# Performance work log

Measured on AMD Instinct MI355X. Metric: run time of the kernel, lower is better.

Reference implementation:

```python
import jax, jax.numpy as jnp
import numpy as np

H = 384          # hidden_dim == filter_size == n_chans
N_BINS = 256
PRED_GRAD = 0.1
LN_EPS = 1e-5


def _conv1d_same(x_bct, w_oik, b):
    k = w_oik.shape[-1]
    p = (k - 1) // 2
    y = jax.lax.conv_general_dilated(
        x_bct, w_oik, window_strides=(1,), padding=[(p, p)],
        dimension_numbers=("NCT", "OIT", "NCT"))
    return y + b[None, :, None]


def _ln_last(x, g, b):  # LayerNorm over last dim
    m = jnp.mean(x, axis=-1, keepdims=True)
    v = jnp.var(x, axis=-1, keepdims=True)
    return (x - m) * jax.lax.rsqrt(v + LN_EPS) * g + b


def _ln_chan(x_bct, g, b):  # LayerNorm over channel dim (dim=1)
    m = jnp.mean(x_bct, axis=1, keepdims=True)
    v = jnp.var(x_bct, axis=1, keepdims=True)
    return (x_bct - m) * jax.lax.rsqrt(v + LN_EPS) * g[None, :, None] + b[None, :, None]


def _sin_pos(x0, dim):
    # fairseq SinusoidalPositionalEmbedding, padding_idx=0, applied to xs[...,0]
    mask = (x0 != 0).astype(jnp.int32)
    pos = jnp.cumsum(mask, axis=1) * mask                        # [B,T]
    half = dim // 2
    inv = jnp.exp(jnp.arange(half, dtype=jnp.float32) * (-(np.log(10000.0) / (half - 1))))
    ang = pos[..., None].astype(jnp.float32) * inv               # [B,T,half]
    pe = jnp.concatenate([jnp.sin(ang), jnp.cos(ang)], axis=-1)  # [B,T,dim]
    return jnp.where(pos[..., None] == 0, 0.0, pe)


def _duration_predictor(x, src_mask, w1, b1, g1, be1, w2, b2, g2, be2, lw, lb):
    h = _conv1d_same(jnp.swapaxes(x, 1, 2), w1, b1)
    h = _ln_last(jax.nn.relu(jnp.swapaxes(h, 1, 2)), g1, be1)
    h = _conv1d_same(jnp.swapaxes(h, 1, 2), w2, b2)
    h = _ln_last(jax.nn.relu(jnp.swapaxes(h, 1, 2)), g2, be2)
    out = (h @ lw + lb)[..., 0]                                  # [B,T]
    return jnp.where(src_mask, 0.0, out)


def _variance_predictor(x, cw, cb, g, b, lw, lb, alpha):
    pos = alpha * _sin_pos(x[..., 0], x.shape[-1])
    h = jnp.swapaxes(x + pos, 1, 2)                              # [B,C,T]
    for i in range(cw.shape[0]):
        h = _ln_chan(jax.nn.relu(_conv1d_same(h, cw[i], cb[i])), g[i], b[i])
    return jnp.swapaxes(h, 1, 2) @ lw + lb                       # [B,T,odim]


def _length_regulate(x, dur_int, max_len):
    B, T, _ = x.shape
    cum = jnp.cumsum(dur_int, axis=1)                            # [B,T]
    frames = jnp.arange(max_len)
    idx = jax.vmap(lambda c: jnp.searchsorted(c, frames, side="right"))(cum)
    idx = jnp.clip(idx, 0, T - 1)                                # [B,max_len]
    out = jnp.take_along_axis(x, idx[..., None], axis=1)         # [B,max_len,H]
    total = cum[:, -1]
    valid = frames[None, :] < total[:, None]
    out = jnp.where(valid[..., None], out, 0.0)
    mel_len = jnp.minimum(total, max_len)
    return out, mel_len


def setup_inputs() -> dict:
    key = jax.random.key(0)
    ks = iter(jax.random.split(key, 40))
    B, T = 32, 1024
    rnd = lambda s: 0.02 * jax.random.normal(next(ks), s, dtype=jnp.float32)
    inp = {
        "x": jax.random.normal(next(ks), (B, T, H), dtype=jnp.float32),
        "src_lens": jax.random.randint(next(ks), (B,), 0, T),
        "src_mask": jnp.zeros((B, T), dtype=bool),
        "max_len": 4096,
        # duration predictor (kernel=3)
        "dp_w1": rnd((H, H, 3)), "dp_b1": jnp.zeros((H,)),
        "dp_ln1_g": jnp.ones((H,)), "dp_ln1_b": jnp.zeros((H,)),
        "dp_w2": rnd((H, H, 3)), "dp_b2": jnp.zeros((H,)),
        "dp_ln2_g": jnp.ones((H,)), "dp_ln2_b": jnp.zeros((H,)),
        "dp_lw": rnd((H, 1)), "dp_lb": jnp.full((1,), 1.5),  # bias -> avg dur ~3.5
        # pitch predictor: 5 layers, kernel=5, odim=1 (use_uv=False)
        "pp_cw": rnd((5, H, H, 5)), "pp_cb": jnp.zeros((5, H)),
        "pp_g": jnp.ones((5, H)), "pp_b": jnp.zeros((5, H)),
        "pp_lw": rnd((H, 1)), "pp_lb": jnp.zeros((1,)), "pp_alpha": jnp.ones((1,)),
        # energy predictor: 2 layers, kernel=5, odim=1
        "ep_cw": rnd((2, H, H, 5)), "ep_cb": jnp.zeros((2, H)),
        "ep_g": jnp.ones((2, H)), "ep_b": jnp.zeros((2, H)),
        "ep_lw": rnd((H, 1)), "ep_lb": jnp.zeros((1,)), "ep_alpha": jnp.ones((1,)),
        # bins (requires_grad=False buffers) + embedding tables
        "pitch_bins": jnp.linspace(-4.0, 4.0, N_BINS - 1),
        "energy_bins": jnp.linspace(-4.0, 4.0, N_BINS - 1),
        "pitch_table": rnd((N_BINS, H)),
        "energy_table": rnd((N_BINS, H)),
    }
    return inp


def reference(x, src_lens, src_mask, max_len,
              dp_w1, dp_b1, dp_ln1_g, dp_ln1_b, dp_w2, dp_b2, dp_ln2_g, dp_ln2_b, dp_lw, dp_lb,
              pp_cw, pp_cb, pp_g, pp_b, pp_lw, pp_lb, pp_alpha,
              ep_cw, ep_cb, ep_g, ep_b, ep_lw, ep_lb, ep_alpha,
              pitch_bins, energy_bins, pitch_table, energy_table):
    # duration (inference path: no targets, controls = 1.0)
    log_d = _duration_predictor(x, src_mask, dp_w1, dp_b1, dp_ln1_g, dp_ln1_b,
                                dp_w2, dp_b2, dp_ln2_g, dp_ln2_b, dp_lw, dp_lb)
    dur = jnp.clip(jnp.round(jnp.exp(log_d) - 1.0), 0.0, None)
    dur_int = dur.astype(jnp.int32)

    # straight-through-style grad scaling on predictor inputs
    xg = jax.lax.stop_gradient(x) + PRED_GRAD * (x - jax.lax.stop_gradient(x))

    # phoneme-level pitch (use_uv=False -> squeeze, bucketize)
    pitch_pred = _variance_predictor(xg, pp_cw, pp_cb, pp_g, pp_b, pp_lw, pp_lb, pp_alpha)[..., 0]
    pitch_idx = jnp.searchsorted(pitch_bins, pitch_pred, side="left")  # torch.bucketize(right=False)
    pitch_emb = pitch_table[pitch_idx]

    # phoneme-level energy
    energy_pred = _variance_predictor(xg, ep_cw, ep_cb, ep_g, ep_b, ep_lw, ep_lb, ep_alpha)[..., 0]
    energy_idx = jnp.searchsorted(energy_bins, energy_pred, side="left")
    energy_emb = energy_table[energy_idx]

    x_adapt = x + pitch_emb + energy_emb
    out, mel_len = _length_regulate(x_adapt, dur_int, int(max_len))
    return out, log_d, dur, pitch_pred, energy_pred, mel_len
```

## Files before the change

kernel.cpp:

```cpp
#include <hip/hip_runtime.h>
#include <cstdint>

#define HH 384
#define NBINS 256

typedef __attribute__((ext_vector_type(8))) short short8v;
typedef __attribute__((ext_vector_type(16))) float f32x16;
typedef __attribute__((ext_vector_type(4))) unsigned short ushort4v;

__device__ inline float4 ld4(const float* p){ return *(const float4*)p; }

__device__ inline unsigned short bf16_rne(float f){
  unsigned u = __float_as_uint(f);
  unsigned r = u + 0x7FFFu + ((u >> 16) & 1u);
  return (unsigned short)(r >> 16);
}
__device__ inline float bf16_to_f(unsigned short h){
  return __uint_as_float(((unsigned)h) << 16);
}

__global__ __launch_bounds__(1024) void pos_kernel(const float* __restrict__ x,
    int* __restrict__ pos, int T)
{
  __shared__ int s[1024];
  int b = blockIdx.x, tid = threadIdx.x;
  int m = 0;
  if (tid < T) m = (x[((size_t)b*T + tid)*HH] != 0.f) ? 1 : 0;
  s[tid] = m;
  __syncthreads();
  for (int off = 1; off < 1024; off <<= 1){
    int add = (tid >= off) ? s[tid-off] : 0;
    __syncthreads();
    s[tid] += add;
    __syncthreads();
  }
  if (tid < T) pos[(size_t)b*T + tid] = s[tid] * m;
}

__global__ __launch_bounds__(HH) void add_pe_kernel(const float* __restrict__ x,
    const int* __restrict__ pos, const float* __restrict__ alpha,
    float* __restrict__ out)
{
  int row = blockIdx.x; int i = threadIdx.x;
  int p = pos[row];
  float pe = 0.f;
  if (p != 0){
    int j = (i < HH/2) ? i : i - HH/2;
    float inv = expf((float)j * -0.04822167734018944f);
    float ang = (float)p * inv;
    pe = (i < HH/2) ? sinf(ang) : cosf(ang);
  }
  out[(size_t)row*HH + i] = x[(size_t)row*HH + i] + alpha[0]*pe;
}

template<int K>
__global__ __launch_bounds__(256) void wtrans_kernel(const float* __restrict__ w,
    unsigned short* __restrict__ dst, int nlayers)
{
  constexpr int SPL = (24*K + 2) * 6144;
  const int per = 384*384;
  int gid = blockIdx.x*256 + threadIdx.x;
  if (gid >= nlayers*per) return;
  int l = gid / per, rem = gid - l*per;
  int o = rem / 384, i = rem - (rem/384)*384;
  unsigned short* whi = dst + (size_t)l*2*SPL;
  unsigned short* wlo = whi + SPL;
  const float* wl = w + (size_t)l*384*384*K;
  int ph = (i >= 192) ? 1 : 0;
  int iloc = i - 192*ph;
  int c = iloc >> 4, half = (iloc >> 3) & 1, jj = iloc & 7;
  #pragma unroll
  for (int k = 0; k < K; ++k){
    float v = wl[((size_t)o*384 + i)*K + k];
    unsigned short hi = bf16_rne(v);
    unsigned short lo = bf16_rne(v - bf16_to_f(hi));
    int s = ph*12*K + k*12 + c;
    size_t d = ((size_t)(s*2 + half)*384 + o)*8 + jj;
    whi[d] = hi; wlo[d] = lo;
  }
}

template<int K>
__global__ __launch_bounds__(256) void conv_mfma_kernel(
    const float* __restrict__ in, const unsigned short* __restrict__ whi,
    const unsigned short* __restrict__ wlo, const float* __restrict__ bias,
    const float* __restrict__ g, const float* __restrict__ be,
    float* __restrict__ out, int T)
{
  constexpr int MT  = 64;
  constexpr int P   = (K-1)/2;
  constexpr int RT  = MT + K - 1;
  constexpr int RA  = RT + 2;
  constexpr int SPH = 12*K;
  constexpr int LDPc = 200;
  __shared__ unsigned short xs_hi[RA*LDPc];
  __shared__ unsigned short xs_lo[RA*LDPc];
  __shared__ float ps[4][64], pq[4][64];

  int ntile = T / MT;
  int b  = blockIdx.x / ntile;
  int t0 = (blockIdx.x % ntile) * MT;
  int tid = threadIdx.x;
  const float* inb = in + (size_t)b*T*HH;

  int wv = tid >> 6, ln = tid & 63;
  int l31 = ln & 31, hl = ln >> 5;
  int o0 = wv * 96;

  f32x16 acc0[3], acc1[3];
  #pragma unroll
  for (int nt = 0; nt < 3; ++nt){
    float bv = bias[o0 + nt*32 + l31];
    #pragma unroll
    for (int r = 0; r < 16; ++r){ acc0[nt][r] = bv; acc1[nt][r] = bv; }
  }

#define GLOAD(dst, p) \
  asm volatile("global_load_dwordx4 %0, %1, off" : "=v"(dst) : "v"(p))

  for (int phse = 0; phse < 2; ++phse){
    if (phse) __syncthreads();

    for (int e4 = tid; e4 < RT*48; e4 += 256){
      int r = e4 / 48, c4 = (e4 - r*48)*4;
      int t = t0 + r - P;
      float4 v = (t >= 0 && t < T) ? ld4(&inb[(size_t)t*HH + phse*192 + c4])
                                   : make_float4(0.f,0.f,0.f,0.f);
      float va[4] = {v.x, v.y, v.z, v.w};
      ushort4v h, l;
      #pragma unroll
      for (int q = 0; q < 4; ++q){
        unsigned short hq = bf16_rne(va[q]);
        h[q] = hq;
        l[q] = bf16_rne(va[q] - bf16_to_f(hq));
      }
      *(ushort4v*)&xs_hi[r*LDPc + c4] = h;
      *(ushort4v*)&xs_lo[r*LDPc + c4] = l;
    }
    __syncthreads();

    const unsigned short* bhp = whi + (size_t)phse*SPH*6144
                                    + ((size_t)hl*384 + o0 + l31)*8;
    const unsigned short* blp = wlo + (size_t)phse*SPH*6144
                                    + ((size_t)hl*384 + o0 + l31)*8;
    int aoff0 = l31*LDPc + hl*8;
    int aoff1 = (32 + l31)*LDPc + hl*8;
    int cc = 0;

    short8v B0h[3], B0l[3], B1h[3], B1l[3];
    short8v A00h, A00l, A01h, A01l;
    short8v A10h, A10l, A11h, A11l;

#define ADVB do{ bhp += 6144; blp += 6144; }while(0)
#define ADVA do{ aoff0 += 16; aoff1 += 16;                                   \
                 if (++cc == 12){ cc = 0; aoff0 += LDPc - 192;               \
                                  aoff1 += LDPc - 192; } }while(0)

    GLOAD(B0h[0], bhp);        GLOAD(B0h[1], bhp + 256); GLOAD(B0h[2], bhp + 512);
    GLOAD(B0l[0], blp);        GLOAD(B0l[1], blp + 256); GLOAD(B0l[2], blp + 512);
    ADVB;
    A00h = *(const short8v*)&xs_hi[aoff0];
    A00l = *(const short8v*)&xs_lo[aoff0];
    A01h = *(const short8v*)&xs_hi[aoff1];
    A01l = *(const short8v*)&xs_lo[aoff1];
    ADVA;

#define STEP(CBh,CBl, CA0h,CA0l,CA1h,CA1l, NBh,NBl, NA0h,NA0l,NA1h,NA1l) do{ \
    GLOAD(NBh[0], bhp);       GLOAD(NBh[1], bhp + 256);                      \
    GLOAD(NBh[2], bhp + 512); GLOAD(NBl[0], blp);                            \
    GLOAD(NBl[1], blp + 256); GLOAD(NBl[2], blp + 512);                      \
    ADVB;                                                                    \
    NA0h = *(const short8v*)&xs_hi[aoff0];                                   \
    NA0l = *(const short8v*)&xs_lo[aoff0];                                   \
    NA1h = *(const short8v*)&xs_hi[aoff1];                                   \
    NA1l = *(const short8v*)&xs_lo[aoff1];                                   \
    ADVA;                                                                    \
    asm volatile("s_waitcnt vmcnt(6)");                                      \
    __builtin_amdgcn_sched_barrier(0);                                       \
    __builtin_amdgcn_s_setprio(1);                                           \
    _Pragma("unroll")                                                        \
    for (int nt = 0; nt < 3; ++nt){                                          \
      acc0[nt] = __builtin_amdgcn_mfma_f32_32x32x16_bf16(CA0h, CBh[nt], acc0[nt], 0,0,0); \
      acc1[nt] = __builtin_amdgcn_mfma_f32_32x32x16_bf16(CA1h, CBh[nt], acc1[nt], 0,0,0); \
    }                                                                        \
    _Pragma("unroll")                                                        \
    for (int nt = 0; nt < 3; ++nt){                                          \
      acc0[nt] = __builtin_amdgcn_mfma_f32_32x32x16_bf16(CA0h, CBl[nt], acc0[nt], 0,0,0); \
      acc1[nt] = __builtin_amdgcn_mfma_f32_32x32x16_bf16(CA1h, CBl[nt], acc1[nt], 0,0,0); \
    }                                                                        \
    _Pragma("unroll")                                                        \
    for (int nt = 0; nt < 3; ++nt){                                          \
      acc0[nt] = __builtin_amdgcn_mfma_f32_32x32x16_bf16(CA0l, CBh[nt], acc0[nt], 0,0,0); \
      acc1[nt] = __builtin_amdgcn_mfma_f32_32x32x16_bf16(CA1l, CBh[nt], acc1[nt], 0,0,0); \
    }                                                                        \
    __builtin_amdgcn_s_setprio(0);                                           \
  } while(0)

    for (int s = 0; s < SPH; s += 2){
      STEP(B0h,B0l, A00h,A00l,A01h,A01l, B1h,B1l, A10h,A10l,A11h,A11l);
      STEP(B1h,B1l, A10h,A10l,A11h,A11l, B0h,B0l, A00h,A00l,A01h,A01l);
    }
#undef STEP
#undef ADVB
#undef ADVA

    asm volatile("s_waitcnt vmcnt(0)");
    __builtin_amdgcn_sched_barrier(0);
  }
#undef GLOAD

  float gv[3], bev[3];
  #pragma unroll
  for (int nt = 0; nt < 3; ++nt){
    gv[nt]  = g[o0 + nt*32 + l31];
    bev[nt] = be[o0 + nt*32 + l31];
  }

  #pragma unroll
  for (int rg = 0; rg < 2; ++rg){
    #pragma unroll
    for (int r = 0; r < 16; ++r){
      float s1 = 0.f, s2 = 0.f;
      #pragma unroll
      for (int nt = 0; nt < 3; ++nt){
        float v = fmaxf(rg ? acc1[nt][r] : acc0[nt][r], 0.f);
        if (rg) acc1[nt][r] = v; else acc0[nt][r] = v;
        s1 += v; s2 += v*v;
      }
      s1 += __shfl_xor(s1, 1);  s2 += __shfl_xor(s2, 1);
      s1 += __shfl_xor(s1, 2);  s2 += __shfl_xor(s2, 2);
      s1 += __shfl_xor(s1, 4);  s2 += __shfl_xor(s2, 4);
      s1 += __shfl_xor(s1, 8);  s2 += __shfl_xor(s2, 8);
      s1 += __shfl_xor(s1, 16); s2 += __shfl_xor(s2, 16);
      if (l31 == 0){
        int t = rg*32 + (r&3) + 8*(r>>2) + 4*hl;
        ps[wv][t] = s1; pq[wv][t] = s2;
      }
    }
  }
  __syncthreads();

  #pragma unroll
  for (int rg = 0; rg < 2; ++rg){
    #pragma unroll
    for (int r = 0; r < 16; ++r){
      int t = rg*32 + (r&3) + 8*(r>>2) + 4*hl;
      float s1 = ps[0][t] + ps[1][t] + ps[2][t] + ps[3][t];
      float s2 = pq[0][t] + pq[1][t] + pq[2][t] + pq[3][t];
      float mn  = s1 * (1.f/HH);
      float var = fmaxf(s2 * (1.f/HH) - mn*mn, 0.f);
      float rr  = rsqrtf(var + 1e-5f);
      float* orow = out + ((size_t)b*T + t0 + t)*HH;
      #pragma unroll
      for (int nt = 0; nt < 3; ++nt){
        float v = rg ? acc1[nt][r] : acc0[nt][r];
        orow[o0 + nt*32 + l31] = (v - mn)*rr*gv[nt] + bev[nt];
      }
    }
  }
}

__global__ __launch_bounds__(256) void proj_var_kernel(const float* __restrict__ h,
    const float* __restrict__ lw, const float* __restrict__ lb,
    const float* __restrict__ bins, float* __restrict__ pred,
    int* __restrict__ idx, int nrows)
{
  int lane = threadIdx.x & 63, wid = threadIdx.x >> 6;
  int wave = blockIdx.x*4 + wid, nw = gridDim.x*4;
  float lwr[6];
  #pragma unroll
  for (int j = 0; j < 6; ++j) lwr[j] = lw[lane + 64*j];
  float lbv = lb[0];
  for (int row = wave; row < nrows; row += nw){
    const float* hr = h + (size_t)row*HH;
    float s = 0.f;
    #pragma unroll
    for (int j = 0; j < 6; ++j) s = fmaf(hr[lane + 64*j], lwr[j], s);
    #pragma unroll
    for (int off = 32; off; off >>= 1) s += __shfl_xor(s, off);
    if (lane == 0){
      float v = s + lbv;
      pred[row] = v;
      int lo = 0, hi = NBINS - 1;
      while (lo < hi){ int mid = (lo + hi) >> 1; if (bins[mid] < v) lo = mid + 1; else hi = mid; }
      idx[row] = lo;
    }
  }
}

__global__ __launch_bounds__(256) void proj_dur_kernel(const float* __restrict__ h,
    const float* __restrict__ lw, const float* __restrict__ lb,
    const unsigned char* __restrict__ mask, float* __restrict__ logd,
    float* __restrict__ durf, int* __restrict__ duri, int nrows)
{
  int lane = threadIdx.x & 63, wid = threadIdx.x >> 6;
  int wave = blockIdx.x*4 + wid, nw = gridDim.x*4;
  float lwr[6];
  #pragma unroll
  for (int j = 0; j < 6; ++j) lwr[j] = lw[lane + 64*j];
  float lbv = lb[0];
  for (int row = wave; row < nrows; row += nw){
    const float* hr = h + (size_t)row*HH;
    float s = 0.f;
    #pragma unroll
    for (int j = 0; j < 6; ++j) s = fmaf(hr[lane + 64*j], lwr[j], s);
    #pragma unroll
    for (int off = 32; off; off >>= 1) s += __shfl_xor(s, off);
    if (lane == 0){
      float v = s + lbv;
      if (mask[row]) v = 0.f;
      logd[row] = v;
      float d = fmaxf(rintf(expf(v) - 1.f), 0.f);
      durf[row] = d;
      duri[row] = (int)d;
    }
  }
}

__global__ __launch_bounds__(1024) void cumsum_kernel(const int* __restrict__ duri,
    int* __restrict__ cum, float* __restrict__ mel, int T, int ML)
{
  __shared__ int s[1024];
  int b = blockIdx.x, tid = threadIdx.x;
  s[tid] = (tid < T) ? duri[(size_t)b*T + tid] : 0;
  __syncthreads();
  for (int off = 1; off < 1024; off <<= 1){
    int add = (tid >= off) ? s[tid-off] : 0;
    __syncthreads();
    s[tid] += add;
    __syncthreads();
  }
  if (tid < T) cum[(size_t)b*T + tid] = s[tid];
  if (tid == T-1) mel[b] = (float)min(s[tid], ML);
}

__global__ __launch_bounds__(256) void xadapt_kernel(const float* __restrict__ x,
    const int* __restrict__ ip, const int* __restrict__ ie,
    const float* __restrict__ pt, const float* __restrict__ et,
    float* __restrict__ xa, int nrows)
{
  int gid = blockIdx.x*256 + threadIdx.x;
  int n4 = nrows * (HH/4);
  if (gid >= n4) return;
  int row = gid / (HH/4);
  int c = gid - row*(HH/4);
  float4 xv = ((const float4*)x)[gid];
  const float4* pr = (const float4*)(pt + (size_t)ip[row]*HH);
  const float4* er = (const float4*)(et + (size_t)ie[row]*HH);
  float4 pv = pr[c], ev = er[c];
  ((float4*)xa)[gid] = make_float4(xv.x+pv.x+ev.x, xv.y+pv.y+ev.y,
                                   xv.z+pv.z+ev.z, xv.w+pv.w+ev.w);
}

__global__ __launch_bounds__(256) void lr_kernel(const float* __restrict__ xa,
    const int* __restrict__ cum, float* __restrict__ out, int T, int ML)
{
  constexpr int FR = 32;
  __shared__ int scum[1024];
  __shared__ int sidx[FR];
  __shared__ int svalid[FR];
  int b  = blockIdx.y;
  int f0 = blockIdx.x * FR;
  for (int i = threadIdx.x; i < T; i += 256) scum[i] = cum[(size_t)b*T + i];
  __syncthreads();
  int total = scum[T-1];
  if (threadIdx.x < FR){
    int f = f0 + threadIdx.x;
    int lo = 0, hi = T;
    while (lo < hi){ int mid = (lo + hi) >> 1; if (scum[mid] <= f) lo = mid + 1; else hi = mid; }
    sidx[threadIdx.x] = min(lo, T-1);
    svalid[threadIdx.x] = (f < total) ? 1 : 0;
  }
  __syncthreads();
  #pragma unroll
  for (int it = 0; it < FR*(HH/4)/256; ++it){
    int item = it*256 + threadIdx.x;
    int fl = item / (HH/4);
    int c  = item - fl*(HH/4);
    int f  = f0 + fl;
    if (f >= ML) continue;
    float4 v = make_float4(0.f,0.f,0.f,0.f);
    if (svalid[fl]) v = ((const float4*)(xa + ((size_t)b*T + sidx[fl])*HH))[c];
    ((float4*)(out + ((size_t)b*ML + f)*HH))[c] = v;
  }
}

extern "C" void kernel_launch(void* const* d_in, const int* in_sizes, int n_in,
                              void* d_out, int out_size, void* d_ws, size_t ws_size,
                              hipStream_t stream)
{
  const float* x        = (const float*)d_in[0];
  const unsigned char* src_mask = (const unsigned char*)d_in[2];
  const float* dp_w1 = (const float*)d_in[4];
  const float* dp_b1 = (const float*)d_in[5];
  const float* dp_g1 = (const float*)d_in[6];
  const float* dp_be1= (const float*)d_in[7];
  const float* dp_w2 = (const float*)d_in[8];
  const float* dp_b2 = (const float*)d_in[9];
  const float* dp_g2 = (const float*)d_in[10];
  const float* dp_be2= (const float*)d_in[11];
  const float* dp_lw = (const float*)d_in[12];
  const float* dp_lb = (const float*)d_in[13];
  const float* pp_cw = (const float*)d_in[14];
  const float* pp_cb = (const float*)d_in[15];
  const float* pp_g  = (const float*)d_in[16];
  const float* pp_b  = (const float*)d_in[17];
  const float* pp_lw = (const float*)d_in[18];
  const float* pp_lb = (const float*)d_in[19];
  const float* pp_alpha = (const float*)d_in[20];
  const float* ep_cw = (const float*)d_in[21];
  const float* ep_cb = (const float*)d_in[22];
  const float* ep_g  = (const float*)d_in[23];
  const float* ep_b  = (const float*)d_in[24];
  const float* ep_lw = (const float*)d_in[25];
  const float* ep_lb = (const float*)d_in[26];
  const float* ep_alpha = (const float*)d_in[27];
  const float* pbins = (const float*)d_in[28];
  const float* ebins = (const float*)d_in[29];
  const float* ptab  = (const float*)d_in[30];
  const float* etab  = (const float*)d_in[31];

  int B = in_sizes[1];
  int T = in_sizes[0] / (B*HH);
  int ML = (int)(((long long)out_size - B - 4LL*B*T) / ((long long)B*HH));
  size_t rows = (size_t)B*T;

  float* bufA = (float*)d_ws;
  float* bufB = bufA + rows*HH;
  int* pos    = (int*)(bufB + rows*HH);
  int* idx_p  = pos + rows;
  int* idx_e  = idx_p + rows;
  int* dur_i  = idx_e + rows;
  int* cum    = dur_i + rows;

  float* out0    = (float*)d_out;
  float* logd    = out0 + (size_t)B*ML*HH;
  float* durf    = logd + rows;
  float* pitchp  = durf + rows;
  float* energyp = pitchp + rows;
  float* mel     = energyp + rows;

  const size_t SPL5 = (size_t)(24*5 + 2)*6144;
  const size_t SPL3 = (size_t)(24*3 + 2)*6144;
  unsigned short* wsc    = (unsigned short*)d_out;
  unsigned short* pitchW = wsc;
  unsigned short* enerW  = pitchW + 5*2*SPL5;
  unsigned short* durW1  = enerW  + 2*2*SPL5;
  unsigned short* durW2  = durW1  + 2*SPL3;

  const int per = 384*384;
  wtrans_kernel<5><<<(5*per + 255)/256, 256, 0, stream>>>(pp_cw, pitchW, 5);
  wtrans_kernel<5><<<(2*per + 255)/256, 256, 0, stream>>>(ep_cw, enerW, 2);
  wtrans_kernel<3><<<(per + 255)/256, 256, 0, stream>>>(dp_w1, durW1, 1);
  wtrans_kernel<3><<<(per + 255)/256, 256, 0, stream>>>(dp_w2, durW2, 1);

  int conv_grid = B * (T / 64);

  pos_kernel<<<B, 1024, 0, stream>>>(x, pos, T);

  add_pe_kernel<<<(int)rows, HH, 0, stream>>>(x, pos, pp_alpha, bufA);
  {
    float* src = bufA; float* dst = bufB;
    for (int l = 0; l < 5; ++l){
      unsigned short* whi = pitchW + (size_t)l*2*SPL5;
      conv_mfma_kernel<5><<<conv_grid, 256, 0, stream>>>(src, whi, whi + SPL5,
          pp_cb + (size_t)l*HH, pp_g + (size_t)l*HH, pp_b + (size_t)l*HH, dst, T);
      float* t2 = dst; dst = src; src = t2;
    }
    proj_var_kernel<<<256, 256, 0, stream>>>(src, pp_lw, pp_lb, pbins,
                                             pitchp, idx_p, (int)rows);
  }

  add_pe_kernel<<<(int)rows, HH, 0, stream>>>(x, pos, ep_alpha, bufA);
  {
    float* src = bufA; float* dst = bufB;
    for (int l = 0; l < 2; ++l){
      unsigned short* whi = enerW + (size_t)l*2*SPL5;
      conv_mfma_kernel<5><<<conv_grid, 256, 0, stream>>>(src, whi, whi + SPL5,
          ep_cb + (size_t)l*HH, ep_g + (size_t)l*HH, ep_b + (size_t)l*HH, dst, T);
      float* t2 = dst; dst = src; src = t2;
    }
    proj_var_kernel<<<256, 256, 0, stream>>>(src, ep_lw, ep_lb, ebins,
                                             energyp, idx_e, (int)rows);
  }

  conv_mfma_kernel<3><<<conv_grid, 256, 0, stream>>>(x, durW1, durW1 + SPL3,
      dp_b1, dp_g1, dp_be1, bufB, T);
  conv_mfma_kernel<3><<<conv_grid, 256, 0, stream>>>(bufB, durW2, durW2 + SPL3,
      dp_b2, dp_g2, dp_be2, bufA, T);
  proj_dur_kernel<<<256, 256, 0, stream>>>(bufA, dp_lw, dp_lb, src_mask,
                                           logd, durf, dur_i, (int)rows);

  cumsum_kernel<<<B, 1024, 0, stream>>>(dur_i, cum, mel, T, ML);

  xadapt_kernel<<<(int)((rows*(HH/4) + 255)/256), 256, 0, stream>>>(
      x, idx_p, idx_e, ptab, etab, bufB, (int)rows);

  lr_kernel<<<dim3(ML/32, B), 256, 0, stream>>>(bufB, cum, out0, T, ML);
}
```

Measured before the change: 1.579 ms.

## Fuse positional embedding, projection heads and x_adapt into conv and regulate kernels

Folds the sinusoidal positional-embedding add into the first conv layer's input staging. The linear projection, bucketize and duration post-processing move into the epilogue of the last conv layer, so that layer's activations are never written out. The pitch/energy embedding add also moves into the length-regulation gather, removing the add_pe, proj and xadapt kernels and their full-tensor round trips through memory. In exchange, the first conv layer now computes a sin/cos per staged element, and the gather kernel reads three rows per output frame.

Measured after the change: 1.371 ms. 1.15x faster.

```diff
diff --git a/kernel.cpp b/kernel.cpp
--- a/kernel.cpp
+++ b/kernel.cpp
@@ -35,22 +35,6 @@
     __syncthreads();
   }
   if (tid < T) pos[(size_t)b*T + tid] = s[tid] * m;
-}
-
-__global__ __launch_bounds__(HH) void add_pe_kernel(const float* __restrict__ x,
-    const int* __restrict__ pos, const float* __restrict__ alpha,
-    float* __restrict__ out)
-{
-  int row = blockIdx.x; int i = threadIdx.x;
-  int p = pos[row];
-  float pe = 0.f;
-  if (p != 0){
-    int j = (i < HH/2) ? i : i - HH/2;
-    float inv = expf((float)j * -0.04822167734018944f);
-    float ang = (float)p * inv;
-    pe = (i < HH/2) ? sinf(ang) : cosf(ang);
-  }
-  out[(size_t)row*HH + i] = x[(size_t)row*HH + i] + alpha[0]*pe;
 }
 
 template<int K>
@@ -80,12 +64,18 @@
   }
 }
 
-template<int K>
+template<int K, int MODE>
 __global__ __launch_bounds__(256) void conv_mfma_kernel(
     const float* __restrict__ in, const unsigned short* __restrict__ whi,
     const unsigned short* __restrict__ wlo, const float* __restrict__ bias,
     const float* __restrict__ g, const float* __restrict__ be,
-    float* __restrict__ out, int T)
+    float* __restrict__ out, int T,
+    const int* __restrict__ posp, const float* __restrict__ alpha,
+    const float* __restrict__ lw, const float* __restrict__ lb,
+    const float* __restrict__ bins, float* __restrict__ pred,
+    int* __restrict__ idx,
+    const unsigned char* __restrict__ mask, float* __restrict__ logd,
+    float* __restrict__ durf, int* __restrict__ duri)
 {
   constexpr int MT  = 64;
   constexpr int P   = (K-1)/2;
@@ -96,6 +86,8 @@
   __shared__ unsigned short xs_hi[RA*LDPc];
   __shared__ unsigned short xs_lo[RA*LDPc];
   __shared__ float ps[4][64], pq[4][64];
+  __shared__ float psP[4][64];
+  __shared__ float sinv[192];
 
   int ntile = T / MT;
   int b  = blockIdx.x / ntile;
@@ -106,6 +98,13 @@
   int wv = tid >> 6, ln = tid & 63;
   int l31 = ln & 31, hl = ln >> 5;
   int o0 = wv * 96;
+
+  float al = 0.f;
+  if constexpr (MODE == 1){
+    al = alpha[0];
+    if (tid < 192) sinv[tid] = expf((float)tid * -0.04822167734018944f);
+    __syncthreads();
+  }
 
   f32x16 acc0[3], acc1[3];
   #pragma unroll
@@ -127,6 +126,18 @@
       float4 v = (t >= 0 && t < T) ? ld4(&inb[(size_t)t*HH + phse*192 + c4])
                                    : make_float4(0.f,0.f,0.f,0.f);
       float va[4] = {v.x, v.y, v.z, v.w};
+      if constexpr (MODE == 1){
+        if (t >= 0 && t < T){
+          int p = posp[(size_t)b*T + t];
+          if (p){
+            #pragma unroll
+            for (int q = 0; q < 4; ++q){
+              float ang = (float)p * sinv[c4 + q];
+              va[q] += al * (phse == 0 ? sinf(ang) : cosf(ang));
+            }
+          }
+        }
+      }
       ushort4v h, l;
       #pragma unroll
       for (int q = 0; q < 4; ++q){
@@ -240,79 +251,68 @@
   }
   __syncthreads();
 
-  #pragma unroll
-  for (int rg = 0; rg < 2; ++rg){
+  if constexpr (MODE <= 1){
     #pragma unroll
-    for (int r = 0; r < 16; ++r){
-      int t = rg*32 + (r&3) + 8*(r>>2) + 4*hl;
-      float s1 = ps[0][t] + ps[1][t] + ps[2][t] + ps[3][t];
-      float s2 = pq[0][t] + pq[1][t] + pq[2][t] + pq[3][t];
-      float mn  = s1 * (1.f/HH);
-      float var = fmaxf(s2 * (1.f/HH) - mn*mn, 0.f);
-      float rr  = rsqrtf(var + 1e-5f);
-      float* orow = out + ((size_t)b*T + t0 + t)*HH;
+    for (int rg = 0; rg < 2; ++rg){
       #pragma unroll
-      for (int nt = 0; nt < 3; ++nt){
-        float v = rg ? acc1[nt][r] : acc0[nt][r];
-        orow[o0 + nt*32 + l31] = (v - mn)*rr*gv[nt] + bev[nt];
-      }
-    }
-  }
-}
-
-__global__ __launch_bounds__(256) void proj_var_kernel(const float* __restrict__ h,
-    const float* __restrict__ lw, const float* __restrict__ lb,
-    const float* __restrict__ bins, float* __restrict__ pred,
-    int* __restrict__ idx, int nrows)
-{
-  int lane = threadIdx.x & 63, wid = threadIdx.x >> 6;
-  int wave = blockIdx.x*4 + wid, nw = gridDim.x*4;
-  float lwr[6];
-  #pragma unroll
-  for (int j = 0; j < 6; ++j) lwr[j] = lw[lane + 64*j];
-  float lbv = lb[0];
-  for (int row = wave; row < nrows; row += nw){
-    const float* hr = h + (size_t)row*HH;
-    float s = 0.f;
+      for (int r = 0; r < 16; ++r){
+        int t = rg*32 + (r&3) + 8*(r>>2) + 4*hl;
+        float s1 = ps[0][t] + ps[1][t] + ps[2][t] + ps[3][t];
+        float s2 = pq[0][t] + pq[1][t] + pq[2][t] + pq[3][t];
+        float mn  = s1 * (1.f/HH);
+        float var = fmaxf(s2 * (1.f/HH) - mn*mn, 0.f);
+        float rr  = rsqrtf(var + 1e-5f);
+        float* orow = out + ((size_t)b*T + t0 + t)*HH;
+        #pragma unroll
+        for (int nt = 0; nt < 3; ++nt){
+          float v = rg ? acc1[nt][r] : acc0[nt][r];
+          orow[o0 + nt*32 + l31] = (v - mn)*rr*gv[nt] + bev[nt];
+        }
+      }
+    }
+  } else {
+    float lwv[3];
     #pragma unroll
-    for (int j = 0; j < 6; ++j) s = fmaf(hr[lane + 64*j], lwr[j], s);
+    for (int nt = 0; nt < 3; ++nt) lwv[nt] = lw[o0 + nt*32 + l31];
     #pragma unroll
-    for (int off = 32; off; off >>= 1) s += __shfl_xor(s, off);
-    if (lane == 0){
-      float v = s + lbv;
-      pred[row] = v;
-      int lo = 0, hi = NBINS - 1;
-      while (lo < hi){ int mid = (lo + hi) >> 1; if (bins[mid] < v) lo = mid + 1; else hi = mid; }
-      idx[row] = lo;
-    }
-  }
-}
-
-__global__ __launch_bounds__(256) void proj_dur_kernel(const float* __restrict__ h,
-    const float* __restrict__ lw, const float* __restrict__ lb,
-    const unsigned char* __restrict__ mask, float* __restrict__ logd,
-    float* __restrict__ durf, int* __restrict__ duri, int nrows)
-{
-  int lane = threadIdx.x & 63, wid = threadIdx.x >> 6;
-  int wave = blockIdx.x*4 + wid, nw = gridDim.x*4;
-  float lwr[6];
-  #pragma unroll
-  for (int j = 0; j < 6; ++j) lwr[j] = lw[lane + 64*j];
-  float lbv = lb[0];
-  for (int row = wave; row < nrows; row += nw){
-    const float* hr = h + (size_t)row*HH;
-    float s = 0.f;
-    #pragma unroll
-    for (int j = 0; j < 6; ++j) s = fmaf(hr[lane + 64*j], lwr[j], s);
-    #pragma unroll
-    for (int off = 32; off; off >>= 1) s += __shfl_xor(s, off);
-    if (lane == 0){
-      float v = s + lbv;
-      if (mask[row]) v = 0.f;
-      logd[row] = v;
-      float d = fmaxf(rintf(expf(v) - 1.f), 0.f);
-      durf[row] = d;
-      duri[row] = (int)d;
+    for (int rg = 0; rg < 2; ++rg){
+      #pragma unroll
+      for (int r = 0; r < 16; ++r){
+        int t = rg*32 + (r&3) + 8*(r>>2) + 4*hl;
+        float s1 = ps[0][t] + ps[1][t] + ps[2][t] + ps[3][t];
+        float s2 = pq[0][t] + pq[1][t] + pq[2][t] + pq[3][t];
+        float mn  = s1 * (1.f/HH);
+        float var = fmaxf(s2 * (1.f/HH) - mn*mn, 0.f);
+        float rr  = rsqrtf(var + 1e-5f);
+        float pv = 0.f;
+        #pragma unroll
+        for (int nt = 0; nt < 3; ++nt){
+          float v = rg ? acc1[nt][r] : acc0[nt][r];
+          pv += ((v - mn)*rr*gv[nt] + bev[nt]) * lwv[nt];
+        }
+        pv += __shfl_xor(pv, 1);  pv += __shfl_xor(pv, 2);
+        pv += __shfl_xor(pv, 4);  pv += __shfl_xor(pv, 8);
+        pv += __shfl_xor(pv, 16);
+        if (l31 == 0) psP[wv][t] = pv;
+      }
+    }
+    __syncthreads();
+    if (tid < MT){
+      float v = psP[0][tid] + psP[1][tid] + psP[2][tid] + psP[3][tid] + lb[0];
+      size_t row = (size_t)b*T + t0 + tid;
+      if constexpr (MODE == 2){
+        pred[row] = v;
+        int lo2 = 0, hi2 = NBINS - 1;
+        while (lo2 < hi2){ int mid = (lo2+hi2) >> 1;
+                           if (bins[mid] < v) lo2 = mid + 1; else hi2 = mid; }
+        idx[row] = lo2;
+      } else {
+        if (mask[row]) v = 0.f;
+        logd[row] = v;
+        float d = fmaxf(rintf(expf(v) - 1.f), 0.f);
+        durf[row] = d;
+        duri[row] = (int)d;
+      }
     }
   }
 }
@@ -334,31 +334,16 @@
   if (tid == T-1) mel[b] = (float)min(s[tid], ML);
 }
 
-__global__ __launch_bounds__(256) void xadapt_kernel(const float* __restrict__ x,
+__global__ __launch_bounds__(256) void lr_kernel(const float* __restrict__ x,
     const int* __restrict__ ip, const int* __restrict__ ie,
     const float* __restrict__ pt, const float* __restrict__ et,
-    float* __restrict__ xa, int nrows)
-{
-  int gid = blockIdx.x*256 + threadIdx.x;
-  int n4 = nrows * (HH/4);
-  if (gid >= n4) return;
-  int row = gid / (HH/4);
-  int c = gid - row*(HH/4);
-  float4 xv = ((const float4*)x)[gid];
-  const float4* pr = (const float4*)(pt + (size_t)ip[row]*HH);
-  const float4* er = (const float4*)(et + (size_t)ie[row]*HH);
-  float4 pv = pr[c], ev = er[c];
-  ((float4*)xa)[gid] = make_float4(xv.x+pv.x+ev.x, xv.y+pv.y+ev.y,
-                                   xv.z+pv.z+ev.z, xv.w+pv.w+ev.w);
-}
-
-__global__ __launch_bounds__(256) void lr_kernel(const float* __restrict__ xa,
     const int* __restrict__ cum, float* __restrict__ out, int T, int ML)
 {
   constexpr int FR = 32;
   __shared__ int scum[1024];
   __shared__ int sidx[FR];
   __shared__ int svalid[FR];
+  __shared__ int sip[FR], sie[FR];
   int b  = blockIdx.y;
   int f0 = blockIdx.x * FR;
   for (int i = threadIdx.x; i < T; i += 256) scum[i] = cum[(size_t)b*T + i];
@@ -368,8 +353,12 @@
     int f = f0 + threadIdx.x;
     int lo = 0, hi = T;
     while (lo < hi){ int mid = (lo + hi) >> 1; if (scum[mid] <= f) lo = mid + 1; else hi = mid; }
-    sidx[threadIdx.x] = min(lo, T-1);
+    int s = min(lo, T-1);
+    sidx[threadIdx.x] = s;
     svalid[threadIdx.x] = (f < total) ? 1 : 0;
+    size_t grow = (size_t)b*T + s;
+    sip[threadIdx.x] = ip[grow];
+    sie[threadIdx.x] = ie[grow];
   }
   __syncthreads();
   #pragma unroll
@@ -380,7 +369,13 @@
     int f  = f0 + fl;
     if (f >= ML) continue;
     float4 v = make_float4(0.f,0.f,0.f,0.f);
-    if (svalid[fl]) v = ((const float4*)(xa + ((size_t)b*T + sidx[fl])*HH))[c];
+    if (svalid[fl]){
+      float4 xv = ((const float4*)(x  + ((size_t)b*T + sidx[fl])*HH))[c];
+      float4 pv = ((const float4*)(pt + (size_t)sip[fl]*HH))[c];
+      float4 ev = ((const float4*)(et + (size_t)sie[fl]*HH))[c];
+      v = make_float4(xv.x+pv.x+ev.x, xv.y+pv.y+ev.y,
+                      xv.z+pv.z+ev.z, xv.w+pv.w+ev.w);
+    }
     ((float4*)(out + ((size_t)b*ML + f)*HH))[c] = v;
   }
 }
@@ -458,43 +453,49 @@
 
   pos_kernel<<<B, 1024, 0, stream>>>(x, pos, T);
 
-  add_pe_kernel<<<(int)rows, HH, 0, stream>>>(x, pos, pp_alpha, bufA);
+#define NOPX nullptr, nullptr
+#define NOPROJ nullptr, nullptr, nullptr, nullptr, nullptr
+#define NODUR  nullptr, nullptr, nullptr, nullptr
+
   {
-    float* src = bufA; float* dst = bufB;
-    for (int l = 0; l < 5; ++l){
+    unsigned short* w0 = pitchW;
+    conv_mfma_kernel<5,1><<<conv_grid, 256, 0, stream>>>(x, w0, w0 + SPL5,
+        pp_cb, pp_g, pp_b, bufB, T, pos, pp_alpha, NOPROJ, NODUR);
+    float* src = bufB; float* dst = bufA;
+    for (int l = 1; l < 4; ++l){
       unsigned short* whi = pitchW + (size_t)l*2*SPL5;
-      conv_mfma_kernel<5><<<conv_grid, 256, 0, stream>>>(src, whi, whi + SPL5,
-          pp_cb + (size_t)l*HH, pp_g + (size_t)l*HH, pp_b + (size_t)l*HH, dst, T);
+      conv_mfma_kernel<5,0><<<conv_grid, 256, 0, stream>>>(src, whi, whi + SPL5,
+          pp_cb + (size_t)l*HH, pp_g + (size_t)l*HH, pp_b + (size_t)l*HH,
+          dst, T, NOPX, NOPROJ, NODUR);
       float* t2 = dst; dst = src; src = t2;
     }
-    proj_var_kernel<<<256, 256, 0, stream>>>(src, pp_lw, pp_lb, pbins,
-                                             pitchp, idx_p, (int)rows);
-  }
-
-  add_pe_kernel<<<(int)rows, HH, 0, stream>>>(x, pos, ep_alpha, bufA);
+    unsigned short* w4 = pitchW + (size_t)4*2*SPL5;
+    conv_mfma_kernel<5,2><<<conv_grid, 256, 0, stream>>>(src, w4, w4 + SPL5,
+        pp_cb + (size_t)4*HH, pp_g + (size_t)4*HH, pp_b + (size_t)4*HH,
+        nullptr, T, NOPX, pp_lw, pp_lb, pbins, pitchp, idx_p, NODUR);
+  }
+
   {
-    float* src = bufA; float* dst = bufB;
-    for (int l = 0; l < 2; ++l){
-      unsigned short* whi = enerW + (size_t)l*2*SPL5;
-      conv_mfma_kernel<5><<<conv_grid, 256, 0, stream>>>(src, whi, whi + SPL5,
-          ep_cb + (size_t)l*HH, ep_g + (size_t)l*HH, ep_b + (size_t)l*HH, dst, T);
-      float* t2 = dst; dst = src; src = t2;
-    }
-    proj_var_kernel<<<256, 256, 0, stream>>>(src, ep_lw, ep_lb, ebins,
-                                             energyp, idx_e, (int)rows);
-  }
-
-  conv_mfma_kernel<3><<<conv_grid, 256, 0, stream>>>(x, durW1, durW1 + SPL3,
-      dp_b1, dp_g1, dp_be1, bufB, T);
-  conv_mfma_kernel<3><<<conv_grid, 256, 0, stream>>>(bufB, durW2, durW2 + SPL3,
-      dp_b2, dp_g2, dp_be2, bufA, T);
-  proj_dur_kernel<<<256, 256, 0, stream>>>(bufA, dp_lw, dp_lb, src_mask,
-                                           logd, durf, dur_i, (int)rows);
+    conv_mfma_kernel<5,1><<<conv_grid, 256, 0, stream>>>(x, enerW, enerW + SPL5,
+        ep_cb, ep_g, ep_b, bufB, T, pos, ep_alpha, NOPROJ, NODUR);
+    unsigned short* w1 = enerW + 2*SPL5;
+    conv_mfma_kernel<5,2><<<conv_grid, 256, 0, stream>>>(bufB, w1, w1 + SPL5,
+        ep_cb + (size_t)HH, ep_g + (size_t)HH, ep_b + (size_t)HH,
+        nullptr, T, NOPX, ep_lw, ep_lb, ebins, energyp, idx_e, NODUR);
+  }
+
+  conv_mfma_kernel<3,0><<<conv_grid, 256, 0, stream>>>(x, durW1, durW1 + SPL3,
+      dp_b1, dp_g1, dp_be1, bufB, T, NOPX, NOPROJ, NODUR);
+  conv_mfma_kernel<3,3><<<conv_grid, 256, 0, stream>>>(bufB, durW2, durW2 + SPL3,
+      dp_b2, dp_g2, dp_be2, nullptr, T, NOPX, dp_lw, dp_lb,
+      nullptr, nullptr, nullptr, src_mask, logd, durf, dur_i);
+
+#undef NOPX
+#undef NOPROJ
+#undef NODUR
 
   cumsum_kernel<<<B, 1024, 0, stream>>>(dur_i, cum, mel, T, ML);
 
-  xadapt_kernel<<<(int)((rows*(HH/4) + 255)/256), 256, 0, stream>>>(
-      x, idx_p, idx_e, ptab, etab, bufB, (int)rows);
-
-  lr_kernel<<<dim3(ML/32, B), 256, 0, stream>>>(bufB, cum, out0, T, ML);
-}
+  lr_kernel<<<dim3(ML/32, B), 256, 0, stream>>>(x, idx_p, idx_e, ptab, etab,
+                                                cum, out0, T, ML);
+}
```
